# Performance work log

Measured on AMD Instinct MI355X. Metric: run time of the kernel, lower is better.

## Reference

```python
import jax, jax.numpy as jnp
import numpy as np

H = 1024      # hidden_size
V = 32000     # output_size (vocab)
L = 128       # max_length (encoder length)
B = 256       # batch


def setup_inputs() -> dict:
    key = jax.random.key(0)
    ks = jax.random.split(key, 16)
    s = 1.0 / np.sqrt(H)
    inp = {
        "input_ids": jax.random.randint(ks[0], (1, B), 0, V),
        "hidden": jax.random.normal(ks[1], (1, B, H), dtype=jnp.float32),
        "encoder_outputs": jax.random.normal(ks[2], (B, L, H), dtype=jnp.float32),
        # parameters
        "emb_table": jax.random.normal(ks[3], (V, H), dtype=jnp.float32),
        "attn_w": jax.random.uniform(ks[4], (L, 2 * H), jnp.float32, -s, s),
        "attn_b": jax.random.uniform(ks[5], (L,), jnp.float32, -s, s),
        "comb_w": jax.random.uniform(ks[6], (H, 2 * H), jnp.float32, -s, s),
        "comb_b": jax.random.uniform(ks[7], (H,), jnp.float32, -s, s),
        "w_ih": jax.random.uniform(ks[8], (3 * H, H), jnp.float32, -s, s),
        "b_ih": jax.random.uniform(ks[9], (3 * H,), jnp.float32, -s, s),
        "w_hh": jax.random.uniform(ks[10], (3 * H, H), jnp.float32, -s, s),
        "b_hh": jax.random.uniform(ks[11], (3 * H,), jnp.float32, -s, s),
        "out_w": jax.random.uniform(ks[12], (V, H), jnp.float32, -s, s),
        "out_b": jax.random.uniform(ks[13], (V,), jnp.float32, -s, s),
    }
    return inp


def reference(input_ids, hidden, encoder_outputs, emb_table,
              attn_w, attn_b, comb_w, comb_b,
              w_ih, b_ih, w_hh, b_hh, out_w, out_b):
    # embedding: input_ids (1, B) -> embedded (1, B, H); dropout is identity in eval
    embedded = emb_table[input_ids]            # (1, B, H)
    emb0 = embedded[0]                         # (B, H)
    h0 = hidden[0]                             # (B, H)

    # Bahdanau-style attention over fixed encoder length L
    attn_logits = jnp.concatenate([emb0, h0], axis=1) @ attn_w.T + attn_b   # (B, L)
    attn_weights = jax.nn.softmax(attn_logits, axis=1)                      # (B, L)
    attn_applied = jnp.einsum("bl,blh->bh", attn_weights, encoder_outputs)  # (B, H)

    # combine + relu
    x = jnp.concatenate([emb0, attn_applied], axis=1) @ comb_w.T + comb_b   # (B, H)
    x = jax.nn.relu(x)

    # single GRU step (PyTorch gate layout: r, z, n)
    gx = x @ w_ih.T + b_ih                     # (B, 3H)
    gh = h0 @ w_hh.T + b_hh                    # (B, 3H)
    xr, xz, xn = jnp.split(gx, 3, axis=1)
    hr, hz, hn = jnp.split(gh, 3, axis=1)
    r = jax.nn.sigmoid(xr + hr)
    z = jax.nn.sigmoid(xz + hz)
    n = jnp.tanh(xn + r * hn)
    h_new = (1.0 - z) * n + z * h0             # (B, H)

    logp = jax.nn.log_softmax(h_new @ out_w.T + out_b, axis=1)   # (B, V)
    return logp, h_new[None], attn_weights
```

## Files before the change

kernel.cpp:

```cpp
#include <hip/hip_runtime.h>
#include <hip/hip_bf16.h>
#include <math.h>

#define H 1024
#define L 128
#define B 256
#define V 32000

typedef __attribute__((ext_vector_type(8))) short bf16x8;
typedef __attribute__((ext_vector_type(4))) float f32x4;

static __device__ __forceinline__ ushort f2bf(float f) {
    unsigned int u = __float_as_uint(f);
    u += 0x7fffu + ((u >> 16) & 1u);
    return (ushort)(u >> 16);
}

__global__ __launch_bounds__(256) void attn_kernel(
    const int* __restrict__ input_ids,
    const float* __restrict__ hidden,
    const float* __restrict__ enc,
    const float* __restrict__ emb_table,
    const float* __restrict__ attn_w,
    const float* __restrict__ attn_b,
    ushort* __restrict__ xcat_b16,
    ushort* __restrict__ h0_b16,
    float* __restrict__ attn_weights_out)
{
    __shared__ float s_e[H];
    __shared__ float s_h[H];
    __shared__ float s_part[256];
    __shared__ float s_w[L];
    __shared__ float s_wr[4];

    const int b = blockIdx.x;
    const int tid = threadIdx.x;

    const int id = input_ids[b];
    const float4* e4 = (const float4*)(emb_table + (size_t)id * H);
    const float4* h4 = (const float4*)(hidden + (size_t)b * H);

    float4 ev = e4[tid];
    float4 hv = h4[tid];
    ((float4*)s_e)[tid] = ev;
    ((float4*)s_h)[tid] = hv;

    {
        uint2 p;
        p.x = (unsigned)f2bf(ev.x) | ((unsigned)f2bf(ev.y) << 16);
        p.y = (unsigned)f2bf(ev.z) | ((unsigned)f2bf(ev.w) << 16);
        *(uint2*)(xcat_b16 + (size_t)b * 2 * H + tid * 4) = p;
        uint2 q;
        q.x = (unsigned)f2bf(hv.x) | ((unsigned)f2bf(hv.y) << 16);
        q.y = (unsigned)f2bf(hv.z) | ((unsigned)f2bf(hv.w) << 16);
        *(uint2*)(h0_b16 + (size_t)b * H + tid * 4) = q;
    }
    __syncthreads();

    const int l = tid & 127;
    const int half = tid >> 7;
    const float4* w4 = (const float4*)(attn_w + (size_t)l * (2 * H) + half * H);
    const float4* s4 = (const float4*)(half ? s_h : s_e);
    float acc = 0.f;
#pragma unroll 4
    for (int k = 0; k < H / 4; ++k) {
        float4 w = w4[k];
        float4 s = s4[k];
        acc += w.x * s.x + w.y * s.y + w.z * s.z + w.w * s.w;
    }
    s_part[tid] = acc;
    __syncthreads();
    if (tid < L) s_w[tid] = s_part[tid] + s_part[tid + 128] + attn_b[tid];
    __syncthreads();

    const int wid = tid >> 6;
    float v = (tid < L) ? s_w[tid] : -INFINITY;
    for (int off = 32; off; off >>= 1) v = fmaxf(v, __shfl_xor(v, off));
    if ((tid & 63) == 0) s_wr[wid] = v;
    __syncthreads();
    const float m = fmaxf(s_wr[0], s_wr[1]);

    float e = 0.f;
    if (tid < L) e = __expf(s_w[tid] - m);
    float sv = e;
    for (int off = 32; off; off >>= 1) sv += __shfl_xor(sv, off);
    __syncthreads();
    if ((tid & 63) == 0) s_wr[wid] = sv;
    __syncthreads();
    const float inv = 1.f / (s_wr[0] + s_wr[1]);
    if (tid < L) {
        float w = e * inv;
        s_w[tid] = w;
        attn_weights_out[(size_t)b * L + tid] = w;
    }
    __syncthreads();

    const float4* enc4 = (const float4*)(enc + (size_t)b * L * H);
    float4 a = {0.f, 0.f, 0.f, 0.f};
#pragma unroll 4
    for (int ll = 0; ll < L; ++ll) {
        const float w = s_w[ll];
        float4 e2 = enc4[(size_t)ll * (H / 4) + tid];
        a.x += w * e2.x; a.y += w * e2.y; a.z += w * e2.z; a.w += w * e2.w;
    }
    {
        uint2 p;
        p.x = (unsigned)f2bf(a.x) | ((unsigned)f2bf(a.y) << 16);
        p.y = (unsigned)f2bf(a.z) | ((unsigned)f2bf(a.w) << 16);
        *(uint2*)(xcat_b16 + (size_t)b * 2 * H + H + tid * 4) = p;
    }
}

template<int K, int MODE>
__global__ __launch_bounds__(256) void mfma_gemm(
    const ushort* __restrict__ A,
    const float* __restrict__ W,
    const float* __restrict__ bias,
    float* __restrict__ outf,
    ushort* __restrict__ outb,
    float* __restrict__ rowsum,
    int N)
{
    constexpr int NT = 32;
    __shared__ ushort sA[256 * 72];
    __shared__ ushort sW[NT * 72];
    __shared__ float sLse[256];

    const int tid = threadIdx.x;
    const int bn = blockIdx.x * NT;
    const int w = tid >> 6;
    const int l = tid & 63;
    const int g = l >> 4;
    const int ln = l & 15;
    const int trow = tid >> 3;
    const int tcol = tid & 7;

    if (MODE == 3) sLse[tid] = __logf(rowsum[tid]);

    f32x4 acc[4][2];
#pragma unroll
    for (int i = 0; i < 4; ++i)
#pragma unroll
        for (int n = 0; n < 2; ++n)
            acc[i][n] = (f32x4){0.f, 0.f, 0.f, 0.f};

    for (int k0 = 0; k0 < K; k0 += 64) {
#pragma unroll
        for (int p = 0; p < 8; ++p) {
            const int r = p * 32 + trow;
            uint4 v = *(const uint4*)(A + (size_t)r * K + k0 + tcol * 8);
            *(uint4*)(sA + r * 72 + tcol * 8) = v;
        }
        {
            const float* wp = W + (size_t)(bn + trow) * K + k0 + tcol * 8;
            float4 w0 = *(const float4*)(wp);
            float4 w1 = *(const float4*)(wp + 4);
            ushort tmp[8];
            tmp[0] = f2bf(w0.x); tmp[1] = f2bf(w0.y); tmp[2] = f2bf(w0.z); tmp[3] = f2bf(w0.w);
            tmp[4] = f2bf(w1.x); tmp[5] = f2bf(w1.y); tmp[6] = f2bf(w1.z); tmp[7] = f2bf(w1.w);
            *(uint4*)(sW + trow * 72 + tcol * 8) = *(const uint4*)tmp;
        }
        __syncthreads();
#pragma unroll
        for (int s = 0; s < 2; ++s) {
            bf16x8 af[4], bfr[2];
#pragma unroll
            for (int i = 0; i < 4; ++i)
                af[i] = *(const bf16x8*)(sA + (64 * w + 16 * i + ln) * 72 + s * 32 + g * 8);
#pragma unroll
            for (int n = 0; n < 2; ++n)
                bfr[n] = *(const bf16x8*)(sW + (16 * n + ln) * 72 + s * 32 + g * 8);
#pragma unroll
            for (int i = 0; i < 4; ++i)
#pragma unroll
                for (int n = 0; n < 2; ++n)
                    acc[i][n] = __builtin_amdgcn_mfma_f32_16x16x32_bf16(af[i], bfr[n], acc[i][n], 0, 0, 0);
        }
        __syncthreads();
    }

    const float b0 = bias[bn + ln];
    const float b1 = bias[bn + 16 + ln];

    if (MODE == 0) {
#pragma unroll
        for (int i = 0; i < 4; ++i)
#pragma unroll
            for (int n = 0; n < 2; ++n)
#pragma unroll
                for (int r = 0; r < 4; ++r)
                    outf[(size_t)(64 * w + 16 * i + 4 * g + r) * N + bn + 16 * n + ln] =
                        acc[i][n][r] + (n ? b1 : b0);
    } else if (MODE == 1) {
#pragma unroll
        for (int i = 0; i < 4; ++i)
#pragma unroll
            for (int n = 0; n < 2; ++n)
#pragma unroll
                for (int r = 0; r < 4; ++r) {
                    float vv = acc[i][n][r] + (n ? b1 : b0);
                    vv = fmaxf(vv, 0.f);
                    outb[(size_t)(64 * w + 16 * i + 4 * g + r) * N + bn + 16 * n + ln] = f2bf(vv);
                }
    } else if (MODE == 2) {
#pragma unroll
        for (int i = 0; i < 4; ++i) {
            float e[4];
#pragma unroll
            for (int r = 0; r < 4; ++r)
                e[r] = __expf(acc[i][0][r] + b0) + __expf(acc[i][1][r] + b1);
#pragma unroll
            for (int msk = 1; msk < 16; msk <<= 1)
#pragma unroll
                for (int r = 0; r < 4; ++r)
                    e[r] += __shfl_xor(e[r], msk);
            if (ln < 4)
                atomicAdd(&rowsum[64 * w + 16 * i + 4 * g + ln], e[ln]);
        }
    } else {
#pragma unroll
        for (int i = 0; i < 4; ++i)
#pragma unroll
            for (int n = 0; n < 2; ++n)
#pragma unroll
                for (int r = 0; r < 4; ++r) {
                    const int row = 64 * w + 16 * i + 4 * g + r;
                    outf[(size_t)row * N + bn + 16 * n + ln] =
                        acc[i][n][r] + (n ? b1 : b0) - sLse[row];
                }
    }
}

__global__ __launch_bounds__(256) void gru_kernel(
    const float* __restrict__ gx,
    const float* __restrict__ gh,
    const float* __restrict__ h0,
    float* __restrict__ h_new,
    ushort* __restrict__ hn_b16,
    float* __restrict__ rowsum)
{
    if (blockIdx.x == 0) rowsum[threadIdx.x] = 0.f;
    const int idx = blockIdx.x * 256 + threadIdx.x;
    const int b = idx >> 10;
    const int j = idx & (H - 1);
    const size_t base = (size_t)b * 3 * H;
    const float xr = gx[base + j];
    const float xz = gx[base + H + j];
    const float xn = gx[base + 2 * H + j];
    const float hr = gh[base + j];
    const float hz = gh[base + H + j];
    const float hn = gh[base + 2 * H + j];
    const float r = 1.f / (1.f + __expf(-(xr + hr)));
    const float z = 1.f / (1.f + __expf(-(xz + hz)));
    const float n = tanhf(xn + r * hn);
    const float out = (1.f - z) * n + z * h0[idx];
    h_new[idx] = out;
    hn_b16[idx] = f2bf(out);
}

extern "C" void kernel_launch(void* const* d_in, const int* in_sizes, int n_in,
                              void* d_out, int out_size, void* d_ws, size_t ws_size,
                              hipStream_t stream) {
    const int*   input_ids = (const int*)d_in[0];
    const float* hidden    = (const float*)d_in[1];
    const float* enc       = (const float*)d_in[2];
    const float* emb_table = (const float*)d_in[3];
    const float* attn_w    = (const float*)d_in[4];
    const float* attn_b    = (const float*)d_in[5];
    const float* comb_w    = (const float*)d_in[6];
    const float* comb_b    = (const float*)d_in[7];
    const float* w_ih      = (const float*)d_in[8];
    const float* b_ih      = (const float*)d_in[9];
    const float* w_hh      = (const float*)d_in[10];
    const float* b_hh      = (const float*)d_in[11];
    const float* out_w     = (const float*)d_in[12];
    const float* out_b     = (const float*)d_in[13];

    float* out = (float*)d_out;
    float* logp         = out;
    float* h_new        = out + (size_t)B * V;
    float* attn_weights = h_new + (size_t)B * H;

    ushort* xcat_b16 = (ushort*)d_ws;
    ushort* h0_b16   = xcat_b16 + (size_t)B * 2 * H;
    ushort* x_b16    = h0_b16 + (size_t)B * H;
    ushort* hn_b16   = x_b16 + (size_t)B * H;
    float*  gx       = (float*)(hn_b16 + (size_t)B * H);
    float*  gh       = gx + (size_t)B * 3 * H;
    float*  rowsum   = gh + (size_t)B * 3 * H;

    attn_kernel<<<dim3(B), dim3(256), 0, stream>>>(
        input_ids, hidden, enc, emb_table, attn_w, attn_b,
        xcat_b16, h0_b16, attn_weights);

    mfma_gemm<2 * H, 1><<<dim3(H / 32), dim3(256), 0, stream>>>(
        xcat_b16, comb_w, comb_b, nullptr, x_b16, nullptr, H);

    mfma_gemm<H, 0><<<dim3(3 * H / 32), dim3(256), 0, stream>>>(
        x_b16, w_ih, b_ih, gx, nullptr, nullptr, 3 * H);

    mfma_gemm<H, 0><<<dim3(3 * H / 32), dim3(256), 0, stream>>>(
        h0_b16, w_hh, b_hh, gh, nullptr, nullptr, 3 * H);

    gru_kernel<<<dim3(B * H / 256), dim3(256), 0, stream>>>(
        gx, gh, hidden, h_new, hn_b16, rowsum);

    mfma_gemm<H, 2><<<dim3(V / 32), dim3(256), 0, stream>>>(
        hn_b16, out_w, out_b, nullptr, nullptr, rowsum, V);

    mfma_gemm<H, 3><<<dim3(V / 32), dim3(256), 0, stream>>>(
        hn_b16, out_w, out_b, logp, nullptr, rowsum, V);
}
```

Measured before the change: 588.2 us.

## Restructure decoder pipeline: fused comb/gh GEMM, single-pass vocab GEMM, swizzled prefetching tiles

The attention kernel now runs 1024 threads per batch row, with split-k dot products and a four-way split of the encoder reduction. The GEMM core gains register prefetch of the next K tile and XOR-swizzled shared memory in place of padding. The combine GEMM and the hidden-to-hidden GEMM share one launch. The vocab projection runs once instead of twice: it writes the logits and accumulates exp sums, and a separate elementwise pass subtracts the log-sum-exp. This avoids recomputing the large output GEMM, at the cost of an extra read and write of the full logit tensor.

```diff
diff --git a/kernel.cpp b/kernel.cpp
--- a/kernel.cpp
+++ b/kernel.cpp
@@ -16,7 +16,7 @@
     return (ushort)(u >> 16);
 }
 
-__global__ __launch_bounds__(256) void attn_kernel(
+__global__ __launch_bounds__(1024) void attn_kernel(
     const int* __restrict__ input_ids,
     const float* __restrict__ hidden,
     const float* __restrict__ enc,
@@ -29,90 +29,244 @@
 {
     __shared__ float s_e[H];
     __shared__ float s_h[H];
-    __shared__ float s_part[256];
     __shared__ float s_w[L];
-    __shared__ float s_wr[4];
+    __shared__ float s_r[4];
+    __shared__ float4 s_pac[3 * 256];
 
     const int b = blockIdx.x;
     const int tid = threadIdx.x;
 
-    const int id = input_ids[b];
-    const float4* e4 = (const float4*)(emb_table + (size_t)id * H);
-    const float4* h4 = (const float4*)(hidden + (size_t)b * H);
-
-    float4 ev = e4[tid];
-    float4 hv = h4[tid];
-    ((float4*)s_e)[tid] = ev;
-    ((float4*)s_h)[tid] = hv;
-
-    {
+    if (tid < 256) {
+        const int id = input_ids[b];
+        float4 ev = ((const float4*)(emb_table + (size_t)id * H))[tid];
+        ((float4*)s_e)[tid] = ev;
         uint2 p;
         p.x = (unsigned)f2bf(ev.x) | ((unsigned)f2bf(ev.y) << 16);
         p.y = (unsigned)f2bf(ev.z) | ((unsigned)f2bf(ev.w) << 16);
         *(uint2*)(xcat_b16 + (size_t)b * 2 * H + tid * 4) = p;
+    } else if (tid < 512) {
+        const int t = tid - 256;
+        float4 hv = ((const float4*)(hidden + (size_t)b * H))[t];
+        ((float4*)s_h)[t] = hv;
         uint2 q;
         q.x = (unsigned)f2bf(hv.x) | ((unsigned)f2bf(hv.y) << 16);
         q.y = (unsigned)f2bf(hv.z) | ((unsigned)f2bf(hv.w) << 16);
-        *(uint2*)(h0_b16 + (size_t)b * H + tid * 4) = q;
-    }
-    __syncthreads();
-
-    const int l = tid & 127;
-    const int half = tid >> 7;
-    const float4* w4 = (const float4*)(attn_w + (size_t)l * (2 * H) + half * H);
-    const float4* s4 = (const float4*)(half ? s_h : s_e);
-    float acc = 0.f;
-#pragma unroll 4
-    for (int k = 0; k < H / 4; ++k) {
-        float4 w = w4[k];
-        float4 s = s4[k];
-        acc += w.x * s.x + w.y * s.y + w.z * s.z + w.w * s.w;
-    }
-    s_part[tid] = acc;
-    __syncthreads();
-    if (tid < L) s_w[tid] = s_part[tid] + s_part[tid + 128] + attn_b[tid];
-    __syncthreads();
-
-    const int wid = tid >> 6;
-    float v = (tid < L) ? s_w[tid] : -INFINITY;
-    for (int off = 32; off; off >>= 1) v = fmaxf(v, __shfl_xor(v, off));
-    if ((tid & 63) == 0) s_wr[wid] = v;
-    __syncthreads();
-    const float m = fmaxf(s_wr[0], s_wr[1]);
-
-    float e = 0.f;
-    if (tid < L) e = __expf(s_w[tid] - m);
-    float sv = e;
-    for (int off = 32; off; off >>= 1) sv += __shfl_xor(sv, off);
-    __syncthreads();
-    if ((tid & 63) == 0) s_wr[wid] = sv;
-    __syncthreads();
-    const float inv = 1.f / (s_wr[0] + s_wr[1]);
-    if (tid < L) {
-        float w = e * inv;
-        s_w[tid] = w;
-        attn_weights_out[(size_t)b * L + tid] = w;
-    }
-    __syncthreads();
-
-    const float4* enc4 = (const float4*)(enc + (size_t)b * L * H);
-    float4 a = {0.f, 0.f, 0.f, 0.f};
-#pragma unroll 4
-    for (int ll = 0; ll < L; ++ll) {
-        const float w = s_w[ll];
-        float4 e2 = enc4[(size_t)ll * (H / 4) + tid];
-        a.x += w * e2.x; a.y += w * e2.y; a.z += w * e2.z; a.w += w * e2.w;
-    }
+        *(uint2*)(h0_b16 + (size_t)b * H + t * 4) = q;
+    }
+    __syncthreads();
+
     {
-        uint2 p;
-        p.x = (unsigned)f2bf(a.x) | ((unsigned)f2bf(a.y) << 16);
-        p.y = (unsigned)f2bf(a.z) | ((unsigned)f2bf(a.w) << 16);
-        *(uint2*)(xcat_b16 + (size_t)b * 2 * H + H + tid * 4) = p;
+        const int ll = tid >> 3;
+        const int p = tid & 7;
+        const float4* wv = (const float4*)(attn_w + (size_t)ll * (2 * H)) + p;
+        const float4* se4 = (const float4*)s_e + p;
+        const float4* sh4 = (const float4*)s_h + p;
+        float acc = 0.f;
+#pragma unroll 8
+        for (int k = 0; k < 32; ++k) {
+            float4 a = wv[k * 8];
+            float4 s = se4[k * 8];
+            acc += a.x * s.x + a.y * s.y + a.z * s.z + a.w * s.w;
+        }
+#pragma unroll 8
+        for (int k = 0; k < 32; ++k) {
+            float4 a = wv[256 + k * 8];
+            float4 s = sh4[k * 8];
+            acc += a.x * s.x + a.y * s.y + a.z * s.z + a.w * s.w;
+        }
+        acc += __shfl_xor(acc, 1);
+        acc += __shfl_xor(acc, 2);
+        acc += __shfl_xor(acc, 4);
+        if (p == 0) s_w[ll] = acc + attn_b[ll];
+    }
+    __syncthreads();
+
+    const int lane = tid & 63;
+    if (tid < 128) {
+        float v = s_w[tid];
+        for (int off = 32; off; off >>= 1) v = fmaxf(v, __shfl_xor(v, off));
+        if (lane == 0) s_r[tid >> 6] = v;
+    }
+    __syncthreads();
+    if (tid < 128) {
+        const float m = fmaxf(s_r[0], s_r[1]);
+        float e = __expf(s_w[tid] - m);
+        float sv = e;
+        for (int off = 32; off; off >>= 1) sv += __shfl_xor(sv, off);
+        if (lane == 0) s_r[2 + (tid >> 6)] = sv;
+        s_w[tid] = e;
+    }
+    __syncthreads();
+    if (tid < 128) {
+        const float inv = 1.f / (s_r[2] + s_r[3]);
+        const float wv = s_w[tid] * inv;
+        s_w[tid] = wv;
+        attn_weights_out[(size_t)b * L + tid] = wv;
+    }
+    __syncthreads();
+
+    {
+        const int grp = tid >> 8;
+        const int c = tid & 255;
+        const float4* enc4 = (const float4*)(enc + (size_t)b * L * H) + c;
+        float ax = 0.f, ay = 0.f, az = 0.f, aw = 0.f;
+#pragma unroll 8
+        for (int q = 0; q < 32; ++q) {
+            const int lidx = grp * 32 + q;
+            const float wv = s_w[lidx];
+            float4 ev = enc4[(size_t)lidx * 256];
+            ax += wv * ev.x; ay += wv * ev.y; az += wv * ev.z; aw += wv * ev.w;
+        }
+        if (grp) {
+            float4 t; t.x = ax; t.y = ay; t.z = az; t.w = aw;
+            s_pac[(grp - 1) * 256 + c] = t;
+        }
+        __syncthreads();
+        if (grp == 0) {
+#pragma unroll
+            for (int j = 0; j < 3; ++j) {
+                float4 t = s_pac[j * 256 + c];
+                ax += t.x; ay += t.y; az += t.z; aw += t.w;
+            }
+            uint2 p;
+            p.x = (unsigned)f2bf(ax) | ((unsigned)f2bf(ay) << 16);
+            p.y = (unsigned)f2bf(az) | ((unsigned)f2bf(aw) << 16);
+            *(uint2*)(xcat_b16 + (size_t)b * 2 * H + H + c * 4) = p;
+        }
     }
 }
 
 template<int K, int MODE>
-__global__ __launch_bounds__(256) void mfma_gemm(
+__device__ __forceinline__ void gemm_core(
+    ushort* sA, ushort* sW,
+    const ushort* __restrict__ A,
+    const float* __restrict__ W,
+    const float* __restrict__ bias,
+    float* __restrict__ outf,
+    ushort* __restrict__ outb,
+    float* __restrict__ rowsum,
+    int N, int bid)
+{
+    const int tid = threadIdx.x;
+    const int bn = bid * 32;
+    const int w = tid >> 6;
+    const int l = tid & 63;
+    const int g = l >> 4;
+    const int ln = l & 15;
+    const int trow = tid >> 3;
+    const int tcol = tid & 7;
+
+    char* sAb = (char*)sA;
+    char* sWb = (char*)sW;
+    const int wsw = (trow & 7) << 4;
+    const int asw = (ln & 7) << 4;
+
+    f32x4 acc[4][2];
+#pragma unroll
+    for (int i = 0; i < 4; ++i)
+#pragma unroll
+        for (int n = 0; n < 2; ++n)
+            acc[i][n] = (f32x4){0.f, 0.f, 0.f, 0.f};
+
+    uint4 pa[8];
+    float4 pw0, pw1;
+    const ushort* arow = A + (size_t)trow * K + tcol * 8;
+    const float* wrow = W + (size_t)(bn + trow) * K + tcol * 8;
+
+    auto LOADT = [&](int k0) {
+#pragma unroll
+        for (int p = 0; p < 8; ++p)
+            pa[p] = *(const uint4*)(arow + (size_t)p * 32 * K + k0);
+        pw0 = *(const float4*)(wrow + k0);
+        pw1 = *(const float4*)(wrow + k0 + 4);
+    };
+    auto STORET = [&]() {
+#pragma unroll
+        for (int p = 0; p < 8; ++p)
+            *(uint4*)(sAb + ((((p * 32 + trow) << 7) + (tcol << 4)) ^ wsw)) = pa[p];
+        ushort t[8];
+        t[0] = f2bf(pw0.x); t[1] = f2bf(pw0.y); t[2] = f2bf(pw0.z); t[3] = f2bf(pw0.w);
+        t[4] = f2bf(pw1.x); t[5] = f2bf(pw1.y); t[6] = f2bf(pw1.z); t[7] = f2bf(pw1.w);
+        *(uint4*)(sWb + (((trow << 7) + (tcol << 4)) ^ wsw)) = *(const uint4*)t;
+    };
+
+    LOADT(0);
+    STORET();
+    __syncthreads();
+
+    for (int k0 = 0; k0 < K; k0 += 64) {
+        if (k0 + 64 < K) LOADT(k0 + 64);
+#pragma unroll
+        for (int s = 0; s < 2; ++s) {
+            bf16x8 af[4], bfr[2];
+#pragma unroll
+            for (int i = 0; i < 4; ++i)
+                af[i] = *(const bf16x8*)(sAb + (((64 * w + 16 * i + ln) << 7) +
+                                               ((s * 64 + (g << 4)) ^ asw)));
+#pragma unroll
+            for (int n = 0; n < 2; ++n)
+                bfr[n] = *(const bf16x8*)(sWb + (((16 * n + ln) << 7) +
+                                                ((s * 64 + (g << 4)) ^ asw)));
+#pragma unroll
+            for (int i = 0; i < 4; ++i)
+#pragma unroll
+                for (int n = 0; n < 2; ++n)
+                    acc[i][n] = __builtin_amdgcn_mfma_f32_16x16x32_bf16(af[i], bfr[n], acc[i][n], 0, 0, 0);
+        }
+        __syncthreads();
+        if (k0 + 64 < K) STORET();
+        __syncthreads();
+    }
+
+    const float b0 = bias[bn + ln];
+    const float b1 = bias[bn + 16 + ln];
+
+    if (MODE == 0) {
+#pragma unroll
+        for (int i = 0; i < 4; ++i)
+#pragma unroll
+            for (int n = 0; n < 2; ++n)
+#pragma unroll
+                for (int r = 0; r < 4; ++r)
+                    outf[(size_t)(64 * w + 16 * i + 4 * g + r) * N + bn + 16 * n + ln] =
+                        acc[i][n][r] + (n ? b1 : b0);
+    } else if (MODE == 1) {
+#pragma unroll
+        for (int i = 0; i < 4; ++i)
+#pragma unroll
+            for (int n = 0; n < 2; ++n)
+#pragma unroll
+                for (int r = 0; r < 4; ++r) {
+                    float vv = acc[i][n][r] + (n ? b1 : b0);
+                    vv = fmaxf(vv, 0.f);
+                    outb[(size_t)(64 * w + 16 * i + 4 * g + r) * N + bn + 16 * n + ln] = f2bf(vv);
+                }
+    } else {
+#pragma unroll
+        for (int i = 0; i < 4; ++i) {
+            float e[4];
+#pragma unroll
+            for (int r = 0; r < 4; ++r) {
+                const float v0 = acc[i][0][r] + b0;
+                const float v1 = acc[i][1][r] + b1;
+                const int row = 64 * w + 16 * i + 4 * g + r;
+                outf[(size_t)row * N + bn + ln] = v0;
+                outf[(size_t)row * N + bn + 16 + ln] = v1;
+                e[r] = __expf(v0) + __expf(v1);
+            }
+#pragma unroll
+            for (int msk = 1; msk < 16; msk <<= 1)
+#pragma unroll
+                for (int r = 0; r < 4; ++r)
+                    e[r] += __shfl_xor(e[r], msk);
+            if (ln < 4)
+                atomicAdd(&rowsum[64 * w + 16 * i + 4 * g + ln], e[ln]);
+        }
+    }
+}
+
+template<int K, int MODE>
+__global__ __launch_bounds__(256, 4) void gemm_kernel(
     const ushort* __restrict__ A,
     const float* __restrict__ W,
     const float* __restrict__ bias,
@@ -121,114 +275,27 @@
     float* __restrict__ rowsum,
     int N)
 {
-    constexpr int NT = 32;
-    __shared__ ushort sA[256 * 72];
-    __shared__ ushort sW[NT * 72];
-    __shared__ float sLse[256];
-
-    const int tid = threadIdx.x;
-    const int bn = blockIdx.x * NT;
-    const int w = tid >> 6;
-    const int l = tid & 63;
-    const int g = l >> 4;
-    const int ln = l & 15;
-    const int trow = tid >> 3;
-    const int tcol = tid & 7;
-
-    if (MODE == 3) sLse[tid] = __logf(rowsum[tid]);
-
-    f32x4 acc[4][2];
-#pragma unroll
-    for (int i = 0; i < 4; ++i)
-#pragma unroll
-        for (int n = 0; n < 2; ++n)
-            acc[i][n] = (f32x4){0.f, 0.f, 0.f, 0.f};
-
-    for (int k0 = 0; k0 < K; k0 += 64) {
-#pragma unroll
-        for (int p = 0; p < 8; ++p) {
-            const int r = p * 32 + trow;
-            uint4 v = *(const uint4*)(A + (size_t)r * K + k0 + tcol * 8);
-            *(uint4*)(sA + r * 72 + tcol * 8) = v;
-        }
-        {
-            const float* wp = W + (size_t)(bn + trow) * K + k0 + tcol * 8;
-            float4 w0 = *(const float4*)(wp);
-            float4 w1 = *(const float4*)(wp + 4);
-            ushort tmp[8];
-            tmp[0] = f2bf(w0.x); tmp[1] = f2bf(w0.y); tmp[2] = f2bf(w0.z); tmp[3] = f2bf(w0.w);
-            tmp[4] = f2bf(w1.x); tmp[5] = f2bf(w1.y); tmp[6] = f2bf(w1.z); tmp[7] = f2bf(w1.w);
-            *(uint4*)(sW + trow * 72 + tcol * 8) = *(const uint4*)tmp;
-        }
-        __syncthreads();
-#pragma unroll
-        for (int s = 0; s < 2; ++s) {
-            bf16x8 af[4], bfr[2];
-#pragma unroll
-            for (int i = 0; i < 4; ++i)
-                af[i] = *(const bf16x8*)(sA + (64 * w + 16 * i + ln) * 72 + s * 32 + g * 8);
-#pragma unroll
-            for (int n = 0; n < 2; ++n)
-                bfr[n] = *(const bf16x8*)(sW + (16 * n + ln) * 72 + s * 32 + g * 8);
-#pragma unroll
-            for (int i = 0; i < 4; ++i)
-#pragma unroll
-                for (int n = 0; n < 2; ++n)
-                    acc[i][n] = __builtin_amdgcn_mfma_f32_16x16x32_bf16(af[i], bfr[n], acc[i][n], 0, 0, 0);
-        }
-        __syncthreads();
-    }
-
-    const float b0 = bias[bn + ln];
-    const float b1 = bias[bn + 16 + ln];
-
-    if (MODE == 0) {
-#pragma unroll
-        for (int i = 0; i < 4; ++i)
-#pragma unroll
-            for (int n = 0; n < 2; ++n)
-#pragma unroll
-                for (int r = 0; r < 4; ++r)
-                    outf[(size_t)(64 * w + 16 * i + 4 * g + r) * N + bn + 16 * n + ln] =
-                        acc[i][n][r] + (n ? b1 : b0);
-    } else if (MODE == 1) {
-#pragma unroll
-        for (int i = 0; i < 4; ++i)
-#pragma unroll
-            for (int n = 0; n < 2; ++n)
-#pragma unroll
-                for (int r = 0; r < 4; ++r) {
-                    float vv = acc[i][n][r] + (n ? b1 : b0);
-                    vv = fmaxf(vv, 0.f);
-                    outb[(size_t)(64 * w + 16 * i + 4 * g + r) * N + bn + 16 * n + ln] = f2bf(vv);
-                }
-    } else if (MODE == 2) {
-#pragma unroll
-        for (int i = 0; i < 4; ++i) {
-            float e[4];
-#pragma unroll
-            for (int r = 0; r < 4; ++r)
-                e[r] = __expf(acc[i][0][r] + b0) + __expf(acc[i][1][r] + b1);
-#pragma unroll
-            for (int msk = 1; msk < 16; msk <<= 1)
-#pragma unroll
-                for (int r = 0; r < 4; ++r)
-                    e[r] += __shfl_xor(e[r], msk);
-            if (ln < 4)
-                atomicAdd(&rowsum[64 * w + 16 * i + 4 * g + ln], e[ln]);
-        }
-    } else {
-#pragma unroll
-        for (int i = 0; i < 4; ++i)
-#pragma unroll
-            for (int n = 0; n < 2; ++n)
-#pragma unroll
-                for (int r = 0; r < 4; ++r) {
-                    const int row = 64 * w + 16 * i + 4 * g + r;
-                    outf[(size_t)row * N + bn + 16 * n + ln] =
-                        acc[i][n][r] + (n ? b1 : b0) - sLse[row];
-                }
-    }
+    __shared__ ushort smem[256 * 64 + 32 * 64];
+    gemm_core<K, MODE>(smem, smem + 256 * 64, A, W, bias, outf, outb, rowsum, N, blockIdx.x);
+}
+
+__global__ __launch_bounds__(256, 4) void comb_gh_kernel(
+    const ushort* __restrict__ xcat,
+    const float* __restrict__ comb_w,
+    const float* __restrict__ comb_b,
+    ushort* __restrict__ x_b16,
+    const ushort* __restrict__ h0b,
+    const float* __restrict__ w_hh,
+    const float* __restrict__ b_hh,
+    float* __restrict__ gh)
+{
+    __shared__ ushort smem[256 * 64 + 32 * 64];
+    if (blockIdx.x < 32)
+        gemm_core<2 * H, 1>(smem, smem + 256 * 64, xcat, comb_w, comb_b,
+                            nullptr, x_b16, nullptr, H, blockIdx.x);
+    else
+        gemm_core<H, 0>(smem, smem + 256 * 64, h0b, w_hh, b_hh,
+                        gh, nullptr, nullptr, 3 * H, blockIdx.x - 32);
 }
 
 __global__ __launch_bounds__(256) void gru_kernel(
@@ -258,6 +325,23 @@
     hn_b16[idx] = f2bf(out);
 }
 
+__global__ __launch_bounds__(256) void logsm_kernel(
+    float* __restrict__ logp,
+    const float* __restrict__ rowsum)
+{
+    __shared__ float s_lse[B];
+    if (threadIdx.x < B) s_lse[threadIdx.x] = __logf(rowsum[threadIdx.x]);
+    __syncthreads();
+    const int total4 = B * V / 4;
+    for (int i = blockIdx.x * 256 + threadIdx.x; i < total4; i += gridDim.x * 256) {
+        float4 v = ((const float4*)logp)[i];
+        const int b = i / (V / 4);
+        const float lse = s_lse[b];
+        v.x -= lse; v.y -= lse; v.z -= lse; v.w -= lse;
+        ((float4*)logp)[i] = v;
+    }
+}
+
 extern "C" void kernel_launch(void* const* d_in, const int* in_sizes, int n_in,
                               void* d_out, int out_size, void* d_ws, size_t ws_size,
                               hipStream_t stream) {
@@ -289,25 +373,21 @@
     float*  gh       = gx + (size_t)B * 3 * H;
     float*  rowsum   = gh + (size_t)B * 3 * H;
 
-    attn_kernel<<<dim3(B), dim3(256), 0, stream>>>(
+    attn_kernel<<<dim3(B), dim3(1024), 0, stream>>>(
         input_ids, hidden, enc, emb_table, attn_w, attn_b,
         xcat_b16, h0_b16, attn_weights);
 
-    mfma_gemm<2 * H, 1><<<dim3(H / 32), dim3(256), 0, stream>>>(
-        xcat_b16, comb_w, comb_b, nullptr, x_b16, nullptr, H);
-
-    mfma_gemm<H, 0><<<dim3(3 * H / 32), dim3(256), 0, stream>>>(
+    comb_gh_kernel<<<dim3(32 + 96), dim3(256), 0, stream>>>(
+        xcat_b16, comb_w, comb_b, x_b16, h0_b16, w_hh, b_hh, gh);
+
+    gemm_kernel<H, 0><<<dim3(3 * H / 32), dim3(256), 0, stream>>>(
         x_b16, w_ih, b_ih, gx, nullptr, nullptr, 3 * H);
-
-    mfma_gemm<H, 0><<<dim3(3 * H / 32), dim3(256), 0, stream>>>(
-        h0_b16, w_hh, b_hh, gh, nullptr, nullptr, 3 * H);
 
     gru_kernel<<<dim3(B * H / 256), dim3(256), 0, stream>>>(
         gx, gh, hidden, h_new, hn_b16, rowsum);
 
-    mfma_gemm<H, 2><<<dim3(V / 32), dim3(256), 0, stream>>>(
-        hn_b16, out_w, out_b, nullptr, nullptr, rowsum, V);
-
-    mfma_gemm<H, 3><<<dim3(V / 32), dim3(256), 0, stream>>>(
+    gemm_kernel<H, 4><<<dim3(V / 32), dim3(256), 0, stream>>>(
         hn_b16, out_w, out_b, logp, nullptr, rowsum, V);
-}
+
+    logsm_kernel<<<dim3(2048), dim3(256), 0, stream>>>(logp, rowsum);
+}
```

Result: slower. 655.6 us (+11.5%).
